# Optimization experiments

Measured on AMD Instinct MI355X. Metric: run time of the kernel, lower is better.

Reference implementation:

```python
import jax, jax.numpy as jnp
import numpy as np

B, T, H = 4, 512, 512          # batch, num_target_nodes, hidden
V = 32000                       # static vocab
S, SDV = 512, 300               # source nodes, source dynamic vocab
TDV = 512                       # target dynamic vocab


def setup_inputs() -> dict:
    key = jax.random.key(0)
    ks = jax.random.split(key, 9)
    src_idx = jax.random.randint(ks[6], (B, S), 0, SDV)
    tgt_idx = jax.random.randint(ks[8], (B, T), 0, TDV)
    return {
        "hiddens": jax.random.normal(ks[0], (B, T, H), jnp.float32),
        "Wp": jax.random.normal(ks[1], (H, 3), jnp.float32) * (1.0 / np.sqrt(H)),
        "bp": jnp.zeros((3,), jnp.float32),
        "Wv": jax.random.normal(ks[2], (H, V), jnp.float32) * (1.0 / np.sqrt(H)),
        "bv": jnp.zeros((V,), jnp.float32),
        "source_attentions": jax.nn.softmax(jax.random.normal(ks[3], (B, T, S), jnp.float32), axis=-1),
        "source_attention_maps": jax.nn.one_hot(src_idx, SDV, dtype=jnp.float32),
        "target_attentions": jax.nn.softmax(jax.random.normal(ks[4], (B, T, TDV), jnp.float32), axis=-1),
        "target_attention_maps": jax.nn.one_hot(tgt_idx, TDV, dtype=jnp.float32),
    }


def reference(hiddens, Wp, bp, Wv, bv, source_attentions, source_attention_maps,
              target_attentions, target_attention_maps):
    b, t, h = hiddens.shape
    hf = hiddens.reshape(b * t, h)
    # switch probabilities: [copy_source, copy_target, generate]
    p = jax.nn.softmax(hf @ Wp + bp, axis=1).reshape(b, t, 3)
    p_copy_source = p[..., 0:1]
    p_copy_target = p[..., 1:2]
    p_generate = p[..., 2:3]
    # vocab scores with pad index masked to -inf (vocab_pad_idx = 0)
    scores = hf @ Wv + bv                      # [b*t, V]
    scores = scores.at[:, 0].set(-jnp.inf)
    vocab_probs = jax.nn.softmax(scores.reshape(b, t, -1), axis=-1)
    scaled_vocab_probs = vocab_probs * p_generate
    # copy distributions via one-hot scatter-sum (dense matmul in original)
    scaled_copy_source_probs = jnp.einsum(
        'bts,bsv->btv', source_attentions * p_copy_source, source_attention_maps)
    scaled_copy_target_probs = jnp.einsum(
        'btn,bnv->btv', target_attentions * p_copy_target, target_attention_maps)
    probs = jnp.concatenate(
        [scaled_vocab_probs, scaled_copy_source_probs, scaled_copy_target_probs], axis=2)
    predictions = jnp.argmax(probs, axis=2)
    return (probs, predictions)
```

## Files before the change

### kernel.cpp

```cpp
#include <hip/hip_runtime.h>
#include <hip/hip_bf16.h>
#include <math.h>

#define Bq   4
#define Tq   512
#define Hq   512
#define Vq   32000
#define Sq   512
#define SDVq 300
#define TDVq 512
#define ROWS (Bq * Tq)
#define OUTW (Vq + SDVq + TDVq)

typedef __bf16 bf16x8 __attribute__((ext_vector_type(8)));
typedef float  fx4    __attribute__((ext_vector_type(4)));

__device__ __forceinline__ void async16(const void* g, void* l) {
    __builtin_amdgcn_global_load_lds(
        (const __attribute__((address_space(1))) void*)g,
        (__attribute__((address_space(3))) void*)l, 16, 0, 0);
}

__global__ void compute_p(const float* __restrict__ hiddens,
                          const float* __restrict__ Wp,
                          const float* __restrict__ bp,
                          float* __restrict__ p) {
    int row  = blockIdx.x;
    int lane = threadIdx.x;
    const float* h = hiddens + (size_t)row * Hq;
    float a0 = 0.f, a1 = 0.f, a2 = 0.f;
    for (int i = lane; i < Hq; i += 64) {
        float hv = h[i];
        a0 += hv * Wp[i * 3 + 0];
        a1 += hv * Wp[i * 3 + 1];
        a2 += hv * Wp[i * 3 + 2];
    }
    for (int off = 32; off > 0; off >>= 1) {
        a0 += __shfl_down(a0, off);
        a1 += __shfl_down(a1, off);
        a2 += __shfl_down(a2, off);
    }
    if (lane == 0) {
        float l0 = a0 + bp[0], l1 = a1 + bp[1], l2 = a2 + bp[2];
        float M  = fmaxf(l0, fmaxf(l1, l2));
        float e0 = expf(l0 - M), e1 = expf(l1 - M), e2 = expf(l2 - M);
        float inv = 1.f / (e0 + e1 + e2);
        p[row * 3 + 0] = e0 * inv;
        p[row * 3 + 1] = e1 * inv;
        p[row * 3 + 2] = e2 * inv;
    }
}

__global__ void extract_idx(const float* __restrict__ map, int ncols,
                            int* __restrict__ idx) {
    int row  = blockIdx.x;
    int lane = threadIdx.x;
    const float* r = map + (size_t)row * ncols;
    float best = -1.f; int bi = 0;
    for (int i = lane; i < ncols; i += 64) {
        float v = r[i];
        if (v > best) { best = v; bi = i; }
    }
    for (int off = 32; off > 0; off >>= 1) {
        float ob  = __shfl_down(best, off);
        int   obi = __shfl_down(bi, off);
        if (ob > best) { best = ob; bi = obi; }
    }
    if (lane == 0) idx[row] = bi;
}

__global__ __launch_bounds__(256)
void convert_a(const float* __restrict__ in, __hip_bfloat16* __restrict__ o) {
    int i = blockIdx.x * 256 + threadIdx.x;
    float4 v = ((const float4*)in)[i];
    __hip_bfloat16* op = o + (size_t)i * 4;
    op[0] = __float2bfloat16(v.x);
    op[1] = __float2bfloat16(v.y);
    op[2] = __float2bfloat16(v.z);
    op[3] = __float2bfloat16(v.w);
}

__global__ __launch_bounds__(256)
void transpose_wv(const float* __restrict__ Wv, __hip_bfloat16* __restrict__ Wt) {
    __shared__ float t[32][33];
    int n0 = blockIdx.x * 32, k0 = blockIdx.y * 32;
    int tx = threadIdx.x, ty = threadIdx.y;
#pragma unroll
    for (int r = 0; r < 4; ++r)
        t[ty + r * 8][tx] = Wv[(size_t)(k0 + ty + r * 8) * Vq + n0 + tx];
    __syncthreads();
#pragma unroll
    for (int r = 0; r < 4; ++r)
        Wt[(size_t)(n0 + ty + r * 8) * Hq + k0 + tx] =
            __float2bfloat16(t[tx][ty + r * 8]);
}

__global__ __launch_bounds__(256)
void gemm_mfma(const __hip_bfloat16* __restrict__ A,
               const __hip_bfloat16* __restrict__ Bt,
               const float* __restrict__ bv,
               float* __restrict__ out) {
    __shared__ __align__(16) unsigned short As[4096];
    __shared__ __align__(16) unsigned short Bs[4096];
    int tid  = threadIdx.x;
    int wave = tid >> 6, lane = tid & 63;
    int bm = blockIdx.x * 128;
    int bn = blockIdx.y * 128;
    int wr = wave >> 1, wc = wave & 1;
    int lr = lane & 15;
    int kq = lane >> 4;

    fx4 acc[4][4];
#pragma unroll
    for (int i = 0; i < 4; ++i)
#pragma unroll
        for (int j = 0; j < 4; ++j)
            acc[i][j] = (fx4){0.f, 0.f, 0.f, 0.f};

    int c0 = tid, c1 = tid + 256;
    int ar0 = c0 & 127, ak0 = (c0 >> 7) * 8;
    int ar1 = c1 & 127, ak1 = (c1 >> 7) * 8;
    const unsigned short* Ag = (const unsigned short*)A;
    const unsigned short* Bg = (const unsigned short*)Bt;
    unsigned short* As0 = &As[(wave << 6) * 8];
    unsigned short* As1 = &As[(256 + (wave << 6)) * 8];
    unsigned short* Bs0 = &Bs[(wave << 6) * 8];
    unsigned short* Bs1 = &Bs[(256 + (wave << 6)) * 8];

    for (int k0 = 0; k0 < Hq; k0 += 32) {
        async16(Ag + (size_t)(bm + ar0) * Hq + k0 + ak0, As0);
        async16(Ag + (size_t)(bm + ar1) * Hq + k0 + ak1, As1);
        async16(Bg + (size_t)(bn + ar0) * Hq + k0 + ak0, Bs0);
        async16(Bg + (size_t)(bn + ar1) * Hq + k0 + ak1, Bs1);
        __syncthreads();

        bf16x8 af[4], bfr[4];
#pragma unroll
        for (int i = 0; i < 4; ++i) {
            int row = wr * 64 + i * 16 + lr;
            af[i] = *(const bf16x8*)&As[(size_t)(kq * 128 + row) * 8];
        }
#pragma unroll
        for (int j = 0; j < 4; ++j) {
            int col = wc * 64 + j * 16 + lr;
            bfr[j] = *(const bf16x8*)&Bs[(size_t)(kq * 128 + col) * 8];
        }
#pragma unroll
        for (int i = 0; i < 4; ++i)
#pragma unroll
            for (int j = 0; j < 4; ++j)
                acc[i][j] = __builtin_amdgcn_mfma_f32_16x16x32_bf16(
                    af[i], bfr[j], acc[i][j], 0, 0, 0);
        __syncthreads();
    }

    float bvv[4];
#pragma unroll
    for (int j = 0; j < 4; ++j)
        bvv[j] = bv[bn + wc * 64 + j * 16 + lr];
#pragma unroll
    for (int i = 0; i < 4; ++i) {
        int gr0 = bm + wr * 64 + i * 16 + kq * 4;
#pragma unroll
        for (int j = 0; j < 4; ++j) {
            int gc = bn + wc * 64 + j * 16 + lr;
#pragma unroll
            for (int r = 0; r < 4; ++r) {
                float v = acc[i][j][r] + bvv[j];
                if (gc == 0) v = -1e30f;
                out[(size_t)(gr0 + r) * OUTW + gc] = v;
            }
        }
    }
}

__global__ __launch_bounds__(256)
void softmax_rows(float* __restrict__ out, const float* __restrict__ p,
                  float* __restrict__ cval, int* __restrict__ cidx) {
    int row = blockIdx.x;
    int tid = threadIdx.x;
    float* rp = out + (size_t)row * OUTW;
    const float4* rv = (const float4*)rp;

    float m = -INFINITY, l = 0.f; int mi = 0;
    for (int i = tid; i < Vq / 4; i += 256) {
        float4 v = rv[i];
        float vv[4] = {v.x, v.y, v.z, v.w};
#pragma unroll
        for (int c = 0; c < 4; ++c) {
            float x = vv[c];
            if (x > m) { l = l * __expf(m - x) + 1.f; m = x; mi = i * 4 + c; }
            else       { l += __expf(x - m); }
        }
    }
    __shared__ float sm[256], sl[256];
    __shared__ int   si[256];
    sm[tid] = m; sl[tid] = l; si[tid] = mi;
    __syncthreads();
    for (int s = 128; s > 0; s >>= 1) {
        if (tid < s) {
            float m1 = sm[tid], l1 = sl[tid]; int i1 = si[tid];
            float m2 = sm[tid + s], l2 = sl[tid + s]; int i2 = si[tid + s];
            float M = fmaxf(m1, m2);
            sl[tid] = l1 * __expf(m1 - M) + l2 * __expf(m2 - M);
            sm[tid] = M;
            si[tid] = (m2 > m1 || (m2 == m1 && i2 < i1)) ? i2 : i1;
        }
        __syncthreads();
    }
    float M = sm[0], L = sl[0];
    float pgen = p[row * 3 + 2];
    float scale = pgen / L;
    if (tid == 0) { cval[row * 3] = scale; cidx[row * 3] = si[0]; }

    float4* wv4 = (float4*)rp;
    for (int i = tid; i < Vq / 4; i += 256) {
        float4 v = rv[i];
        v.x = __expf(v.x - M) * scale;
        v.y = __expf(v.y - M) * scale;
        v.z = __expf(v.z - M) * scale;
        v.w = __expf(v.w - M) * scale;
        wv4[i] = v;
    }
}

__global__ __launch_bounds__(256)
void copy_scatter(const float* __restrict__ att, const int* __restrict__ idx,
                  const float* __restrict__ p, int pcol, int slot,
                  int natt, int nout, float* __restrict__ out, int out_off,
                  float* __restrict__ cval, int* __restrict__ cidx) {
    int row = blockIdx.x;
    int b   = row >> 9;
    int tid = threadIdx.x;
    __shared__ float acc[TDVq];
    for (int i = tid; i < nout; i += 256) acc[i] = 0.f;
    __syncthreads();
    const float* arow = att + (size_t)row * natt;
    const int*   ib   = idx + b * natt;
    for (int s = tid; s < natt; s += 256) {
        atomicAdd(&acc[ib[s]], arow[s]);
    }
    __syncthreads();
    float pc = p[row * 3 + pcol];
    float* orow = out + (size_t)row * OUTW + out_off;
    float bm_ = -INFINITY; int bi = 0;
    for (int v = tid; v < nout; v += 256) {
        float val = acc[v] * pc;
        orow[v] = val;
        if (val > bm_) { bm_ = val; bi = v; }
    }
    __shared__ float bs[256];
    __shared__ int   is_[256];
    bs[tid] = bm_; is_[tid] = bi;
    __syncthreads();
    for (int s = 128; s > 0; s >>= 1) {
        if (tid < s) {
            float v2 = bs[tid + s]; int i2 = is_[tid + s];
            if (v2 > bs[tid] || (v2 == bs[tid] && i2 < is_[tid])) {
                bs[tid] = v2; is_[tid] = i2;
            }
        }
        __syncthreads();
    }
    if (tid == 0) { cval[row * 3 + slot] = bs[0]; cidx[row * 3 + slot] = out_off + is_[0]; }
}

__global__ void combine_pred(const float* __restrict__ cval,
                             const int* __restrict__ cidx,
                             float* __restrict__ pred) {
    int r = blockIdx.x * 256 + threadIdx.x;
    if (r >= ROWS) return;
    float v = cval[r * 3]; int i = cidx[r * 3];
    if (cval[r * 3 + 1] > v) { v = cval[r * 3 + 1]; i = cidx[r * 3 + 1]; }
    if (cval[r * 3 + 2] > v) { v = cval[r * 3 + 2]; i = cidx[r * 3 + 2]; }
    pred[r] = (float)i;
}

extern "C" void kernel_launch(void* const* d_in, const int* in_sizes, int n_in,
                              void* d_out, int out_size, void* d_ws, size_t ws_size,
                              hipStream_t stream) {
    const float* hiddens = (const float*)d_in[0];
    const float* Wp      = (const float*)d_in[1];
    const float* bp      = (const float*)d_in[2];
    const float* Wv      = (const float*)d_in[3];
    const float* bv      = (const float*)d_in[4];
    const float* src_att = (const float*)d_in[5];
    const float* src_map = (const float*)d_in[6];
    const float* tgt_att = (const float*)d_in[7];
    const float* tgt_map = (const float*)d_in[8];

    float* out  = (float*)d_out;
    float* pred = out + (size_t)ROWS * OUTW;

    char* ws = (char*)d_ws;
    float* p_ws   = (float*)(ws);
    int*   sidx   = (int*)(ws + (24 << 10));
    int*   tidx   = (int*)(ws + (32 << 10));
    float* cval   = (float*)(ws + (40 << 10));
    int*   cidx   = (int*)(ws + (64 << 10));
    __hip_bfloat16* A_bf = (__hip_bfloat16*)(ws + (128 << 10));
    __hip_bfloat16* Wt   = (__hip_bfloat16*)(ws + (128 << 10) + (2 << 20));

    convert_a<<<ROWS * Hq / 4 / 256, 256, 0, stream>>>(hiddens, A_bf);
    {
        dim3 tg(Vq / 32, Hq / 32);
        dim3 tb(32, 8);
        transpose_wv<<<tg, tb, 0, stream>>>(Wv, Wt);
    }

    compute_p<<<ROWS, 64, 0, stream>>>(hiddens, Wp, bp, p_ws);
    extract_idx<<<Bq * Sq, 64, 0, stream>>>(src_map, SDVq, sidx);
    extract_idx<<<Bq * Tq, 64, 0, stream>>>(tgt_map, TDVq, tidx);

    {
        dim3 gg(ROWS / 128, Vq / 128);
        gemm_mfma<<<gg, 256, 0, stream>>>(A_bf, Wt, bv, out);
    }

    softmax_rows<<<ROWS, 256, 0, stream>>>(out, p_ws, cval, cidx);

    copy_scatter<<<ROWS, 256, 0, stream>>>(src_att, sidx, p_ws, 0, 1, Sq, SDVq,
                                           out, Vq, cval, cidx);
    copy_scatter<<<ROWS, 256, 0, stream>>>(tgt_att, tidx, p_ws, 1, 2, TDVq, TDVq,
                                           out, Vq + SDVq, cval, cidx);

    combine_pred<<<(ROWS + 255) / 256, 256, 0, stream>>>(cval, cidx, pred);
}
```

Measured before the change: 656.9 us.

## Fuse softmax max/sum partials into GEMM epilogue and pipeline loads via registers

The GEMM epilogue now computes per-tile row max, argmax and exp-sum partials and writes them to workspace. A small row_stats kernel merges them, and a finalize pass applies exp and scale in one read-write sweep. This replaces the softmax kernel's two full reads of the 32000-wide rows. The GEMM also swaps async global-to-LDS loads for register-staged double-buffered loads with an XOR-swizzled LDS layout to cut bank conflicts. The cost is extra workspace traffic for the partials and one more kernel launch.

```diff
diff --git a/kernel.cpp b/kernel.cpp
--- a/kernel.cpp
+++ b/kernel.cpp
@@ -11,15 +11,10 @@
 #define TDVq 512
 #define ROWS (Bq * Tq)
 #define OUTW (Vq + SDVq + TDVq)
+#define NBLK 250
 
 typedef __bf16 bf16x8 __attribute__((ext_vector_type(8)));
 typedef float  fx4    __attribute__((ext_vector_type(4)));
-
-__device__ __forceinline__ void async16(const void* g, void* l) {
-    __builtin_amdgcn_global_load_lds(
-        (const __attribute__((address_space(1))) void*)g,
-        (__attribute__((address_space(3))) void*)l, 16, 0, 0);
-}
 
 __global__ void compute_p(const float* __restrict__ hiddens,
                           const float* __restrict__ Wp,
@@ -96,19 +91,29 @@
 }
 
 __global__ __launch_bounds__(256)
-void gemm_mfma(const __hip_bfloat16* __restrict__ A,
-               const __hip_bfloat16* __restrict__ Bt,
+void gemm_mfma(const unsigned short* __restrict__ A,
+               const unsigned short* __restrict__ Bt,
                const float* __restrict__ bv,
-               float* __restrict__ out) {
+               float* __restrict__ out,
+               float* __restrict__ pm, float* __restrict__ pl,
+               int* __restrict__ pc) {
     __shared__ __align__(16) unsigned short As[4096];
     __shared__ __align__(16) unsigned short Bs[4096];
-    int tid  = threadIdx.x;
-    int wave = tid >> 6, lane = tid & 63;
-    int bm = blockIdx.x * 128;
-    int bn = blockIdx.y * 128;
-    int wr = wave >> 1, wc = wave & 1;
-    int lr = lane & 15;
-    int kq = lane >> 4;
+    const int tid  = threadIdx.x;
+    const int wave = tid >> 6, lane = tid & 63;
+    const int bnIdx = blockIdx.y;
+    const int bm = blockIdx.x * 128;
+    const int bn = bnIdx * 128;
+    const int wr = wave >> 1, wc = wave & 1;
+    const int lr = lane & 15, kq = lane >> 4;
+
+    const int c0 = tid, c1 = tid + 256;
+    const size_t gA0 = (size_t)(bm + (c0 >> 2)) * Hq + (c0 & 3) * 8;
+    const size_t gA1 = (size_t)(bm + (c1 >> 2)) * Hq + (c1 & 3) * 8;
+    const size_t gB0 = (size_t)(bn + (c0 >> 2)) * Hq + (c0 & 3) * 8;
+    const size_t gB1 = (size_t)(bn + (c1 >> 2)) * Hq + (c1 & 3) * 8;
+    const int lA0 = (c0 >> 2) * 32 + (((c0 & 3) ^ ((c0 >> 2) & 3)) * 8);
+    const int lA1 = (c1 >> 2) * 32 + (((c1 & 3) ^ ((c1 >> 2) & 3)) * 8);
 
     fx4 acc[4][4];
 #pragma unroll
@@ -117,110 +122,163 @@
         for (int j = 0; j < 4; ++j)
             acc[i][j] = (fx4){0.f, 0.f, 0.f, 0.f};
 
-    int c0 = tid, c1 = tid + 256;
-    int ar0 = c0 & 127, ak0 = (c0 >> 7) * 8;
-    int ar1 = c1 & 127, ak1 = (c1 >> 7) * 8;
-    const unsigned short* Ag = (const unsigned short*)A;
-    const unsigned short* Bg = (const unsigned short*)Bt;
-    unsigned short* As0 = &As[(wave << 6) * 8];
-    unsigned short* As1 = &As[(256 + (wave << 6)) * 8];
-    unsigned short* Bs0 = &Bs[(wave << 6) * 8];
-    unsigned short* Bs1 = &Bs[(256 + (wave << 6)) * 8];
-
-    for (int k0 = 0; k0 < Hq; k0 += 32) {
-        async16(Ag + (size_t)(bm + ar0) * Hq + k0 + ak0, As0);
-        async16(Ag + (size_t)(bm + ar1) * Hq + k0 + ak1, As1);
-        async16(Bg + (size_t)(bn + ar0) * Hq + k0 + ak0, Bs0);
-        async16(Bg + (size_t)(bn + ar1) * Hq + k0 + ak1, Bs1);
+    uint4 sa[2][2], sb[2][2];
+    sa[0][0] = *(const uint4*)(A + gA0);
+    sa[0][1] = *(const uint4*)(A + gA1);
+    sb[0][0] = *(const uint4*)(Bt + gB0);
+    sb[0][1] = *(const uint4*)(Bt + gB1);
+    sa[1][0] = *(const uint4*)(A + gA0 + 32);
+    sa[1][1] = *(const uint4*)(A + gA1 + 32);
+    sb[1][0] = *(const uint4*)(Bt + gB0 + 32);
+    sb[1][1] = *(const uint4*)(Bt + gB1 + 32);
+
+    const int permB = (kq ^ (lr & 3)) * 8;
+
+#pragma unroll
+    for (int it = 0; it < 16; ++it) {
+        const int st = it & 1;
         __syncthreads();
-
+        *(uint4*)&As[lA0] = sa[st][0];
+        *(uint4*)&As[lA1] = sa[st][1];
+        *(uint4*)&Bs[lA0] = sb[st][0];
+        *(uint4*)&Bs[lA1] = sb[st][1];
+        __syncthreads();
+        const int kn = (it + 2) * 32;
+        if (kn < Hq) {
+            sa[st][0] = *(const uint4*)(A + gA0 + kn);
+            sa[st][1] = *(const uint4*)(A + gA1 + kn);
+            sb[st][0] = *(const uint4*)(Bt + gB0 + kn);
+            sb[st][1] = *(const uint4*)(Bt + gB1 + kn);
+        }
         bf16x8 af[4], bfr[4];
 #pragma unroll
-        for (int i = 0; i < 4; ++i) {
-            int row = wr * 64 + i * 16 + lr;
-            af[i] = *(const bf16x8*)&As[(size_t)(kq * 128 + row) * 8];
-        }
-#pragma unroll
-        for (int j = 0; j < 4; ++j) {
-            int col = wc * 64 + j * 16 + lr;
-            bfr[j] = *(const bf16x8*)&Bs[(size_t)(kq * 128 + col) * 8];
-        }
+        for (int i = 0; i < 4; ++i)
+            af[i] = *(const bf16x8*)&As[(wr * 64 + i * 16 + lr) * 32 + permB];
+#pragma unroll
+        for (int j = 0; j < 4; ++j)
+            bfr[j] = *(const bf16x8*)&Bs[(wc * 64 + j * 16 + lr) * 32 + permB];
 #pragma unroll
         for (int i = 0; i < 4; ++i)
 #pragma unroll
             for (int j = 0; j < 4; ++j)
                 acc[i][j] = __builtin_amdgcn_mfma_f32_16x16x32_bf16(
                     af[i], bfr[j], acc[i][j], 0, 0, 0);
-        __syncthreads();
     }
 
     float bvv[4];
 #pragma unroll
     for (int j = 0; j < 4; ++j)
         bvv[j] = bv[bn + wc * 64 + j * 16 + lr];
+
+    __syncthreads();
+    float* sM = (float*)As;
+    float* sL = sM + 256;
+    int*   sC = (int*)Bs;
+
 #pragma unroll
     for (int i = 0; i < 4; ++i) {
-        int gr0 = bm + wr * 64 + i * 16 + kq * 4;
-#pragma unroll
-        for (int j = 0; j < 4; ++j) {
-            int gc = bn + wc * 64 + j * 16 + lr;
-#pragma unroll
-            for (int r = 0; r < 4; ++r) {
-                float v = acc[i][j][r] + bvv[j];
-                if (gc == 0) v = -1e30f;
-                out[(size_t)(gr0 + r) * OUTW + gc] = v;
+        int rbase = wr * 64 + i * 16 + kq * 4;
+#pragma unroll
+        for (int r = 0; r < 4; ++r) {
+            int rloc = rbase + r;
+            float v[4];
+            float m = -INFINITY; int c = 0x7fffffff;
+#pragma unroll
+            for (int j = 0; j < 4; ++j) {
+                int gc = bn + wc * 64 + j * 16 + lr;
+                float x = acc[i][j][r] + bvv[j];
+                if (gc == 0) x = -1e30f;
+                v[j] = x;
+                out[(size_t)(bm + rloc) * OUTW + gc] = x;
+                if (x > m) { m = x; c = gc; }
+            }
+#pragma unroll
+            for (int off = 1; off < 16; off <<= 1) {
+                float om = __shfl_xor(m, off);
+                int   oc = __shfl_xor(c, off);
+                if (om > m || (om == m && oc < c)) { m = om; c = oc; }
+            }
+            float l = 0.f;
+#pragma unroll
+            for (int j = 0; j < 4; ++j) l += __expf(v[j] - m);
+#pragma unroll
+            for (int off = 1; off < 16; off <<= 1)
+                l += __shfl_xor(l, off);
+            if (lr == 0) {
+                sM[rloc * 2 + wc] = m;
+                sL[rloc * 2 + wc] = l;
+                sC[rloc * 2 + wc] = c;
             }
         }
     }
-}
-
-__global__ __launch_bounds__(256)
-void softmax_rows(float* __restrict__ out, const float* __restrict__ p,
-                  float* __restrict__ cval, int* __restrict__ cidx) {
+    __syncthreads();
+    if (tid < 128) {
+        float m0 = sM[tid * 2], m1 = sM[tid * 2 + 1];
+        float l0 = sL[tid * 2], l1 = sL[tid * 2 + 1];
+        int   cc0 = sC[tid * 2], cc1 = sC[tid * 2 + 1];
+        float M = fmaxf(m0, m1);
+        float L = l0 * __expf(m0 - M) + l1 * __expf(m1 - M);
+        int   C = (m1 > m0 || (m1 == m0 && cc1 < cc0)) ? cc1 : cc0;
+        size_t o = (size_t)(bm + tid) * 256 + bnIdx;
+        pm[o] = M; pl[o] = L; pc[o] = C;
+    }
+}
+
+__global__ __launch_bounds__(256)
+void row_stats(const float* __restrict__ pm, const float* __restrict__ pl,
+               const int* __restrict__ pc, const float* __restrict__ p,
+               float* __restrict__ rowM, float* __restrict__ rowScale,
+               float* __restrict__ cval, int* __restrict__ cidx) {
+    int wave = threadIdx.x >> 6, lane = threadIdx.x & 63;
+    int row  = blockIdx.x * 4 + wave;
+    const float* pmr = pm + (size_t)row * 256;
+    const float* plr = pl + (size_t)row * 256;
+    const int*   pcr = pc + (size_t)row * 256;
+    float m[4], l[4]; int c[4];
+#pragma unroll
+    for (int t = 0; t < 4; ++t) {
+        int i = lane + t * 64;
+        if (i < NBLK) { m[t] = pmr[i]; l[t] = plr[i]; c[t] = pcr[i]; }
+        else          { m[t] = -INFINITY; l[t] = 0.f; c[t] = 0x7fffffff; }
+    }
+    float M = m[0]; int C = c[0];
+#pragma unroll
+    for (int t = 1; t < 4; ++t)
+        if (m[t] > M || (m[t] == M && c[t] < C)) { M = m[t]; C = c[t]; }
+#pragma unroll
+    for (int off = 1; off < 64; off <<= 1) {
+        float om = __shfl_xor(M, off);
+        int   oc = __shfl_xor(C, off);
+        if (om > M || (om == M && oc < C)) { M = om; C = oc; }
+    }
+    float Lp = 0.f;
+#pragma unroll
+    for (int t = 0; t < 4; ++t) Lp += l[t] * __expf(m[t] - M);
+#pragma unroll
+    for (int off = 1; off < 64; off <<= 1) Lp += __shfl_xor(Lp, off);
+    if (lane == 0) {
+        float pgen  = p[row * 3 + 2];
+        float scale = pgen / Lp;
+        rowM[row] = M; rowScale[row] = scale;
+        cval[row * 3] = scale;
+        cidx[row * 3] = C;
+    }
+}
+
+__global__ __launch_bounds__(256)
+void finalize(float* __restrict__ out, const float* __restrict__ rowM,
+              const float* __restrict__ rowScale) {
     int row = blockIdx.x;
-    int tid = threadIdx.x;
-    float* rp = out + (size_t)row * OUTW;
-    const float4* rv = (const float4*)rp;
-
-    float m = -INFINITY, l = 0.f; int mi = 0;
-    for (int i = tid; i < Vq / 4; i += 256) {
-        float4 v = rv[i];
-        float vv[4] = {v.x, v.y, v.z, v.w};
-#pragma unroll
-        for (int c = 0; c < 4; ++c) {
-            float x = vv[c];
-            if (x > m) { l = l * __expf(m - x) + 1.f; m = x; mi = i * 4 + c; }
-            else       { l += __expf(x - m); }
-        }
-    }
-    __shared__ float sm[256], sl[256];
-    __shared__ int   si[256];
-    sm[tid] = m; sl[tid] = l; si[tid] = mi;
-    __syncthreads();
-    for (int s = 128; s > 0; s >>= 1) {
-        if (tid < s) {
-            float m1 = sm[tid], l1 = sl[tid]; int i1 = si[tid];
-            float m2 = sm[tid + s], l2 = sl[tid + s]; int i2 = si[tid + s];
-            float M = fmaxf(m1, m2);
-            sl[tid] = l1 * __expf(m1 - M) + l2 * __expf(m2 - M);
-            sm[tid] = M;
-            si[tid] = (m2 > m1 || (m2 == m1 && i2 < i1)) ? i2 : i1;
-        }
-        __syncthreads();
-    }
-    float M = sm[0], L = sl[0];
-    float pgen = p[row * 3 + 2];
-    float scale = pgen / L;
-    if (tid == 0) { cval[row * 3] = scale; cidx[row * 3] = si[0]; }
-
-    float4* wv4 = (float4*)rp;
-    for (int i = tid; i < Vq / 4; i += 256) {
-        float4 v = rv[i];
-        v.x = __expf(v.x - M) * scale;
-        v.y = __expf(v.y - M) * scale;
-        v.z = __expf(v.z - M) * scale;
-        v.w = __expf(v.w - M) * scale;
-        wv4[i] = v;
+    float M = rowM[row], s = rowScale[row];
+    float4* rp = (float4*)(out + (size_t)row * OUTW);
+    int half = blockIdx.y * 4000;
+    for (int i = threadIdx.x + half; i < half + 4000; i += 256) {
+        float4 v = rp[i];
+        v.x = __expf(v.x - M) * s;
+        v.y = __expf(v.y - M) * s;
+        v.z = __expf(v.z - M) * s;
+        v.w = __expf(v.w - M) * s;
+        rp[i] = v;
     }
 }
 
@@ -293,13 +351,18 @@
     float* pred = out + (size_t)ROWS * OUTW;
 
     char* ws = (char*)d_ws;
-    float* p_ws   = (float*)(ws);
-    int*   sidx   = (int*)(ws + (24 << 10));
-    int*   tidx   = (int*)(ws + (32 << 10));
-    float* cval   = (float*)(ws + (40 << 10));
-    int*   cidx   = (int*)(ws + (64 << 10));
-    __hip_bfloat16* A_bf = (__hip_bfloat16*)(ws + (128 << 10));
-    __hip_bfloat16* Wt   = (__hip_bfloat16*)(ws + (128 << 10) + (2 << 20));
+    float* p_ws     = (float*)(ws);
+    int*   sidx     = (int*)(ws + (24 << 10));
+    int*   tidx     = (int*)(ws + (32 << 10));
+    float* cval     = (float*)(ws + (40 << 10));
+    int*   cidx     = (int*)(ws + (64 << 10));
+    float* rowM     = (float*)(ws + (88 << 10));
+    float* rowScale = (float*)(ws + (96 << 10));
+    float* pm_ws    = (float*)(ws + (128 << 10));
+    float* pl_ws    = (float*)(ws + (128 << 10) + (2 << 20));
+    int*   pc_ws    = (int*)  (ws + (128 << 10) + (4 << 20));
+    __hip_bfloat16* A_bf = (__hip_bfloat16*)(ws + (128 << 10) + (6 << 20));
+    __hip_bfloat16* Wt   = (__hip_bfloat16*)(ws + (128 << 10) + (8 << 20));
 
     convert_a<<<ROWS * Hq / 4 / 256, 256, 0, stream>>>(hiddens, A_bf);
     {
@@ -313,11 +376,18 @@
     extract_idx<<<Bq * Tq, 64, 0, stream>>>(tgt_map, TDVq, tidx);
 
     {
-        dim3 gg(ROWS / 128, Vq / 128);
-        gemm_mfma<<<gg, 256, 0, stream>>>(A_bf, Wt, bv, out);
-    }
-
-    softmax_rows<<<ROWS, 256, 0, stream>>>(out, p_ws, cval, cidx);
+        dim3 gg(ROWS / 128, NBLK);
+        gemm_mfma<<<gg, 256, 0, stream>>>((const unsigned short*)A_bf,
+                                          (const unsigned short*)Wt, bv, out,
+                                          pm_ws, pl_ws, pc_ws);
+    }
+
+    row_stats<<<ROWS / 4, 256, 0, stream>>>(pm_ws, pl_ws, pc_ws, p_ws,
+                                            rowM, rowScale, cval, cidx);
+    {
+        dim3 fg(ROWS, 2);
+        finalize<<<fg, 256, 0, stream>>>(out, rowM, rowScale);
+    }
 
     copy_scatter<<<ROWS, 256, 0, stream>>>(src_att, sidx, p_ws, 0, 1, Sq, SDVq,
                                            out, Vq, cval, cidx);
```

Result: slower. 855.4 us (+30.2%).
